# Performance work log

Hardware: AMD Instinct MI355X
Metric: run time of the kernel (lower is better)

## Reference

```python
import jax, jax.numpy as jnp
import numpy as np

H = 16          # num_heads
TOP_K = 2
LN_EPS = 1e-5


def setup_inputs() -> dict:
    key = jax.random.key(0)
    ks = jax.random.split(key, 8)
    B, S, E, NE = 2, 1024, 1024, 8
    w = lambda k, shp: jax.random.normal(k, shp, dtype=jnp.float32) * 0.02
    return {
        "x": jax.random.normal(ks[0], (B, S, E), dtype=jnp.float32),
        "rW1": w(ks[1], (E // 2, E)),
        "rb1": jnp.zeros((E // 2,), jnp.float32),
        "ln_g": jnp.ones((E // 2,), jnp.float32),
        "ln_b": jnp.zeros((E // 2,), jnp.float32),
        "rW2": w(ks[2], (NE, E // 2)),
        "rb2": jnp.zeros((NE,), jnp.float32),
        "qW": w(ks[3], (NE, E, E)),
        "qb": jnp.zeros((NE, E), jnp.float32),
        "kW": w(ks[4], (NE, E, E)),
        "kb": jnp.zeros((NE, E), jnp.float32),
        "vW": w(ks[5], (NE, E, E)),
        "vb": jnp.zeros((NE, E), jnp.float32),
        "oW": w(ks[6], (NE, E, E)),
        "ob": jnp.zeros((NE, E), jnp.float32),
    }


def reference(x, rW1, rb1, ln_g, ln_b, rW2, rb2, qW, qb, kW, kb, vW, vb, oW, ob):
    B, S, E = x.shape
    NE = qW.shape[0]
    Dh = E // H
    scale = 1.0 / jnp.sqrt(jnp.asarray(Dh, x.dtype))

    # ---- router: Linear -> LayerNorm -> ReLU -> Linear ----
    h = x @ rW1.T + rb1                       # [B,S,E/2]
    mu = h.mean(-1, keepdims=True)
    var = ((h - mu) ** 2).mean(-1, keepdims=True)
    h = (h - mu) * jax.lax.rsqrt(var + LN_EPS) * ln_g + ln_b
    h = jax.nn.relu(h)
    logits = h @ rW2.T + rb2                  # [B,S,NE]
    probs = jax.nn.softmax(logits, axis=-1)

    # ---- top-k gating, renormalized, scattered to dense expert mask ----
    tp, ti = jax.lax.top_k(probs, TOP_K)      # [B,S,K]
    tp = tp / tp.sum(-1, keepdims=True)
    expert_mask = (jax.nn.one_hot(ti, NE, dtype=probs.dtype) * tp[..., None]).sum(-2)  # [B,S,NE]
    gates = jnp.moveaxis(expert_mask, -1, 0)  # [NE,B,S]

    # ---- every expert attends over all tokens; outputs gated and summed ----
    def expert_step(acc, params):
        qw, qb_, kw, kb_, vw, vb_, ow, ob_, g = params
        q = (x @ qw.T + qb_).reshape(B, S, H, Dh).transpose(0, 2, 1, 3)  # [B,H,S,Dh]
        k = (x @ kw.T + kb_).reshape(B, S, H, Dh).transpose(0, 2, 1, 3)
        v = (x @ vw.T + vb_).reshape(B, S, H, Dh).transpose(0, 2, 1, 3)
        scores = jnp.einsum("bhqd,bhkd->bhqk", q, k) * scale
        p = jax.nn.softmax(scores, axis=-1)
        o = jnp.einsum("bhqk,bhkd->bhqd", p, v)
        o = o.transpose(0, 2, 1, 3).reshape(B, S, E) @ ow.T + ob_
        return acc + o * g[..., None], None

    out, _ = jax.lax.scan(expert_step, jnp.zeros_like(x),
                          (qW, qb, kW, kb, vW, vb, oW, ob, gates))
    return out
```

## Files before the change

kernel.cpp:

```cpp
#include <hip/hip_runtime.h>
#include <hip/hip_bf16.h>

typedef unsigned short u16;
typedef unsigned int u32;
typedef __bf16 bf16x8 __attribute__((ext_vector_type(8)));
typedef float f32x4 __attribute__((ext_vector_type(4)));

__device__ __forceinline__ u16 f2bf(float f) {
  union { float f; unsigned u; } v; v.f = f;
  unsigned r = v.u + 0x7fffu + ((v.u >> 16) & 1u);
  return (u16)(r >> 16);
}

__device__ __forceinline__ f32x4 mfma16(bf16x8 a, bf16x8 b, f32x4 c) {
  return __builtin_amdgcn_mfma_f32_16x16x32_bf16(a, b, c, 0, 0, 0);
}

__device__ __forceinline__ void gl_lds16(const u16* g, u16* l) {
  __builtin_amdgcn_global_load_lds(
      (const __attribute__((address_space(1))) u32*)g,
      (__attribute__((address_space(3))) u32*)l, 16, 0, 0);
}

__global__ __launch_bounds__(256) void cvt_x_kernel(const float* __restrict__ x,
                                                    u16* __restrict__ xb,
                                                    u32* __restrict__ lists) {
  size_t i = (size_t)blockIdx.x * 256 + threadIdx.x;
  if (i < 32784) lists[i] = 0;
  float4 v = reinterpret_cast<const float4*>(x)[i];
  unsigned long long pk = (unsigned long long)f2bf(v.x) |
                          ((unsigned long long)f2bf(v.y) << 16) |
                          ((unsigned long long)f2bf(v.z) << 32) |
                          ((unsigned long long)f2bf(v.w) << 48);
  *reinterpret_cast<unsigned long long*>(xb + i * 4) = pk;
}

__global__ __launch_bounds__(256) void cvt_w_kernel(
    const float* __restrict__ qW, const float* __restrict__ kW,
    const float* __restrict__ vW, const float* __restrict__ oW,
    u16* __restrict__ wb_qkv, u16* __restrict__ wb_o) {
  const size_t nqkv4 = (size_t)8 * 3 * 262144;
  const size_t total = nqkv4 + (size_t)8 * 262144;
  for (size_t i = (size_t)blockIdx.x * 256 + threadIdx.x; i < total;
       i += (size_t)gridDim.x * 256) {
    const float* src; u16* dst;
    if (i < nqkv4) {
      size_t elem = i * 4;
      size_t blk = elem >> 20;
      size_t el = blk / 3, ty = blk % 3;
      const float* W = (ty == 0 ? qW : (ty == 1 ? kW : vW));
      src = W + el * 1048576 + (elem & 1048575);
      dst = wb_qkv + elem;
    } else {
      size_t elem = (i - nqkv4) * 4;
      size_t el = elem >> 20;
      src = oW + el * 1048576 + (elem & 1048575);
      dst = wb_o + elem;
    }
    float4 v = *reinterpret_cast<const float4*>(src);
    unsigned long long pk = (unsigned long long)f2bf(v.x) |
                            ((unsigned long long)f2bf(v.y) << 16) |
                            ((unsigned long long)f2bf(v.z) << 32) |
                            ((unsigned long long)f2bf(v.w) << 48);
    *reinterpret_cast<unsigned long long*>(dst) = pk;
  }
}

__global__ __launch_bounds__(256) void router_gemm1(
    const float* __restrict__ x, const float* __restrict__ rW1,
    const float* __restrict__ rb1, float* __restrict__ hbuf) {
  __shared__ float aT[32][72];
  __shared__ float bT[32][72];
  int t = threadIdx.x;
  int tx = t & 15, ty = t >> 4;
  int m0 = blockIdx.x * 64, n0 = blockIdx.y * 64;
  float acc[4][4];
#pragma unroll
  for (int i = 0; i < 4; ++i)
#pragma unroll
    for (int j = 0; j < 4; ++j) acc[i][j] = 0.f;
  const float* Ab = x + (size_t)m0 * 1024;
  const float* Bb = rW1 + (size_t)n0 * 1024;
  int r = t >> 2, c8 = (t & 3) * 8;
  for (int k0 = 0; k0 < 1024; k0 += 32) {
    float4 av0 = *reinterpret_cast<const float4*>(Ab + (size_t)r * 1024 + k0 + c8);
    float4 av1 = *reinterpret_cast<const float4*>(Ab + (size_t)r * 1024 + k0 + c8 + 4);
    float4 bv0 = *reinterpret_cast<const float4*>(Bb + (size_t)r * 1024 + k0 + c8);
    float4 bv1 = *reinterpret_cast<const float4*>(Bb + (size_t)r * 1024 + k0 + c8 + 4);
    aT[c8 + 0][r] = av0.x; aT[c8 + 1][r] = av0.y; aT[c8 + 2][r] = av0.z; aT[c8 + 3][r] = av0.w;
    aT[c8 + 4][r] = av1.x; aT[c8 + 5][r] = av1.y; aT[c8 + 6][r] = av1.z; aT[c8 + 7][r] = av1.w;
    bT[c8 + 0][r] = bv0.x; bT[c8 + 1][r] = bv0.y; bT[c8 + 2][r] = bv0.z; bT[c8 + 3][r] = bv0.w;
    bT[c8 + 4][r] = bv1.x; bT[c8 + 5][r] = bv1.y; bT[c8 + 6][r] = bv1.z; bT[c8 + 7][r] = bv1.w;
    __syncthreads();
#pragma unroll
    for (int kk = 0; kk < 32; ++kk) {
      float4 a = *reinterpret_cast<const float4*>(&aT[kk][ty * 4]);
      float4 b = *reinterpret_cast<const float4*>(&bT[kk][tx * 4]);
      float aa[4] = {a.x, a.y, a.z, a.w};
      float bb[4] = {b.x, b.y, b.z, b.w};
#pragma unroll
      for (int i = 0; i < 4; ++i)
#pragma unroll
        for (int j = 0; j < 4; ++j) acc[i][j] += aa[i] * bb[j];
    }
    __syncthreads();
  }
#pragma unroll
  for (int i = 0; i < 4; ++i) {
    int row = m0 + ty * 4 + i;
#pragma unroll
    for (int j = 0; j < 4; ++j) {
      int col = n0 + tx * 4 + j;
      hbuf[(size_t)row * 512 + col] = acc[i][j] + rb1[col];
    }
  }
}

__global__ __launch_bounds__(64) void router_finish(
    const float* __restrict__ hbuf, const float* __restrict__ ln_g,
    const float* __restrict__ ln_b, const float* __restrict__ rW2,
    const float* __restrict__ rb2,
    u32* __restrict__ tok_list, float* __restrict__ gate_list,
    u32* __restrict__ cnt, u32* __restrict__ inv) {
  int tok = blockIdx.x, lane = threadIdx.x;
  const float* hr = hbuf + (size_t)tok * 512;
  float4 v0 = *reinterpret_cast<const float4*>(hr + lane * 8);
  float4 v1 = *reinterpret_cast<const float4*>(hr + lane * 8 + 4);
  float hv[8] = {v0.x, v0.y, v0.z, v0.w, v1.x, v1.y, v1.z, v1.w};
  float s = 0.f;
#pragma unroll
  for (int j = 0; j < 8; ++j) s += hv[j];
#pragma unroll
  for (int m = 1; m < 64; m <<= 1) s += __shfl_xor(s, m);
  float mu = s * (1.0f / 512.0f);
  float s2 = 0.f;
#pragma unroll
  for (int j = 0; j < 8; ++j) { float d = hv[j] - mu; s2 += d * d; }
#pragma unroll
  for (int m = 1; m < 64; m <<= 1) s2 += __shfl_xor(s2, m);
  float rstd = 1.0f / sqrtf(s2 * (1.0f / 512.0f) + 1e-5f);
#pragma unroll
  for (int j = 0; j < 8; ++j) {
    float tv = (hv[j] - mu) * rstd * ln_g[lane * 8 + j] + ln_b[lane * 8 + j];
    hv[j] = fmaxf(tv, 0.0f);
  }
  float logit[8];
#pragma unroll
  for (int n = 0; n < 8; ++n) {
    const float* wr = rW2 + (size_t)n * 512 + lane * 8;
    float p = 0.f;
#pragma unroll
    for (int j = 0; j < 8; ++j) p += hv[j] * wr[j];
#pragma unroll
    for (int m = 1; m < 64; m <<= 1) p += __shfl_xor(p, m);
    logit[n] = p + rb2[n];
  }
  int i1 = 0; float l1 = logit[0];
#pragma unroll
  for (int n = 1; n < 8; ++n) if (logit[n] > l1) { l1 = logit[n]; i1 = n; }
  int i2 = -1; float l2 = -3.4e38f;
#pragma unroll
  for (int n = 0; n < 8; ++n) if (n != i1 && logit[n] > l2) { l2 = logit[n]; i2 = n; }
  float e2 = __expf(l2 - l1);
  float g1 = 1.0f / (1.0f + e2);
  float g2 = e2 * g1;
  if (lane == 0) {
    int b = tok >> 10, sq = tok & 1023;
    int p1 = i1 * 2 + b;
    u32 pos1 = atomicAdd(&cnt[p1], 1u);
    tok_list[p1 * 1024 + pos1] = (u32)sq;
    gate_list[p1 * 1024 + pos1] = g1;
    inv[tok * 2 + 0] = ((u32)p1 << 10) | pos1;
    int p2 = i2 * 2 + b;
    u32 pos2 = atomicAdd(&cnt[p2], 1u);
    tok_list[p2 * 1024 + pos2] = (u32)sq;
    gate_list[p2 * 1024 + pos2] = g2;
    inv[tok * 2 + 1] = ((u32)p2 << 10) | pos2;
  }
}

__device__ __forceinline__ void stage8(
    const u16* aS0, const u16* aS1, const u16* aS2, const u16* aS3,
    const u16* bS0, const u16* bS1, const u16* bS2, const u16* bS3,
    int k0, u16* aL, u16* bL, int w) {
  gl_lds16(aS0 + k0, aL + (32 * w + 0) * 64);
  gl_lds16(aS1 + k0, aL + (32 * w + 8) * 64);
  gl_lds16(aS2 + k0, aL + (32 * w + 16) * 64);
  gl_lds16(aS3 + k0, aL + (32 * w + 24) * 64);
  gl_lds16(bS0 + k0, bL + (32 * w + 0) * 64);
  gl_lds16(bS1 + k0, bL + (32 * w + 8) * 64);
  gl_lds16(bS2 + k0, bL + (32 * w + 16) * 64);
  gl_lds16(bS3 + k0, bL + (32 * w + 24) * 64);
}

__device__ __forceinline__ void gemm_mainloop_p(
    const u16* aS0, const u16* aS1, const u16* aS2, const u16* aS3,
    const u16* bS0, const u16* bS1, const u16* bS2, const u16* bS3,
    int K, u16* aL0, u16* bL0, u16* aL1, u16* bL1, f32x4 acc[4][4]) {
  const int t = threadIdx.x;
  const int w = t >> 6, lane = t & 63;
  const int wm = (w >> 1) * 64, wn = (w & 1) * 64;
  const int lr = lane & 15, lg = lane >> 4;
  const int T = K >> 6;
  stage8(aS0, aS1, aS2, aS3, bS0, bS1, bS2, bS3, 0, aL0, bL0, w);
  __syncthreads();
  for (int tt = 0; tt < T; ++tt) {
    u16* aC = (tt & 1) ? aL1 : aL0;
    u16* bC = (tt & 1) ? bL1 : bL0;
    if (tt + 1 < T) {
      u16* aN = (tt & 1) ? aL0 : aL1;
      u16* bN = (tt & 1) ? bL0 : bL1;
      stage8(aS0, aS1, aS2, aS3, bS0, bS1, bS2, bS3, (tt + 1) << 6, aN, bN, w);
    }
    __builtin_amdgcn_s_setprio(1);
#pragma unroll
    for (int kk = 0; kk < 2; ++kk) {
      bf16x8 af[4], bfr[4];
#pragma unroll
      for (int i = 0; i < 4; ++i) {
        int ra = wm + i * 16 + lr;
        af[i] = *reinterpret_cast<const bf16x8*>(aC + ra * 64 + (((kk * 4 + lg) ^ (ra & 7)) << 3));
        int rb = wn + i * 16 + lr;
        bfr[i] = *reinterpret_cast<const bf16x8*>(bC + rb * 64 + (((kk * 4 + lg) ^ (rb & 7)) << 3));
      }
#pragma unroll
      for (int mi = 0; mi < 4; ++mi)
#pragma unroll
        for (int ni = 0; ni < 4; ++ni)
          acc[mi][ni] = mfma16(af[mi], bfr[ni], acc[mi][ni]);
    }
    __builtin_amdgcn_s_setprio(0);
    __syncthreads();
  }
}

__device__ __forceinline__ void stage6(
    const u16* aS0, const u16* aS1,
    const u16* bS0, const u16* bS1, const u16* bS2, const u16* bS3,
    int k0, u16* aL, u16* bL, int w) {
  gl_lds16(aS0 + k0, aL + (16 * w + 0) * 64);
  gl_lds16(aS1 + k0, aL + (16 * w + 8) * 64);
  gl_lds16(bS0 + k0, bL + (32 * w + 0) * 64);
  gl_lds16(bS1 + k0, bL + (32 * w + 8) * 64);
  gl_lds16(bS2 + k0, bL + (32 * w + 16) * 64);
  gl_lds16(bS3 + k0, bL + (32 * w + 24) * 64);
}

__device__ __forceinline__ void gemm_mainloop64(
    const u16* aS0, const u16* aS1,
    const u16* bS0, const u16* bS1, const u16* bS2, const u16* bS3,
    int K, u16* aL0, u16* bL0, u16* aL1, u16* bL1, f32x4 acc[4][2]) {
  const int t = threadIdx.x;
  const int w = t >> 6, lane = t & 63;
  const int lr = lane & 15, lg = lane >> 4;
  const int T = K >> 6;
  stage6(aS0, aS1, bS0, bS1, bS2, bS3, 0, aL0, bL0, w);
  __syncthreads();
  for (int tt = 0; tt < T; ++tt) {
    u16* aC = (tt & 1) ? aL1 : aL0;
    u16* bC = (tt & 1) ? bL1 : bL0;
    if (tt + 1 < T) {
      u16* aN = (tt & 1) ? aL0 : aL1;
      u16* bN = (tt & 1) ? bL0 : bL1;
      stage6(aS0, aS1, bS0, bS1, bS2, bS3, (tt + 1) << 6, aN, bN, w);
    }
    __builtin_amdgcn_s_setprio(1);
#pragma unroll
    for (int kk = 0; kk < 2; ++kk) {
      bf16x8 af[4], bfr[2];
#pragma unroll
      for (int i = 0; i < 4; ++i) {
        int ra = i * 16 + lr;
        af[i] = *reinterpret_cast<const bf16x8*>(aC + ra * 64 + (((kk * 4 + lg) ^ (ra & 7)) << 3));
      }
#pragma unroll
      for (int j = 0; j < 2; ++j) {
        int rb = w * 32 + j * 16 + lr;
        bfr[j] = *reinterpret_cast<const bf16x8*>(bC + rb * 64 + (((kk * 4 + lg) ^ (rb & 7)) << 3));
      }
#pragma unroll
      for (int mi = 0; mi < 4; ++mi)
#pragma unroll
        for (int ni = 0; ni < 2; ++ni)
          acc[mi][ni] = mfma16(af[mi], bfr[ni], acc[mi][ni]);
    }
    __builtin_amdgcn_s_setprio(0);
    __syncthreads();
  }
}

__global__ __launch_bounds__(256) void kv_gemm_kernel(
    const u16* __restrict__ xb, const u16* __restrict__ wb_qkv,
    const float* __restrict__ kb, const float* __restrict__ vb,
    u16* __restrict__ kbuf, u16* __restrict__ vtbuf) {
  __shared__ u16 lds[32768];
  int orig = blockIdx.x;
  int wgid = (orig & 7) * 256 + (orig >> 3);
  int e = wgid >> 8, r = wgid & 255;
  int ty = r >> 7, rr = r & 127;
  const int t = threadIdx.x, w = t >> 6, lane = t & 63;
  const int rloc = lane >> 3, cloc = lane & 7;
  const int sc8 = (cloc ^ rloc) * 8;
  const u16 *A, *B;
  int mblk, nblk;
  if (ty == 0) {
    mblk = rr >> 3; nblk = rr & 7;
    A = xb + (size_t)mblk * 128 * 1024;
    B = wb_qkv + (size_t)(e * 3 + 1) * 1048576 + (size_t)nblk * 128 * 1024;
  } else {
    mblk = rr & 7; nblk = rr >> 3;
    A = wb_qkv + (size_t)(e * 3 + 2) * 1048576 + (size_t)mblk * 128 * 1024;
    B = xb + (size_t)nblk * 128 * 1024;
  }
  f32x4 acc[4][4];
#pragma unroll
  for (int i = 0; i < 4; ++i)
#pragma unroll
    for (int j = 0; j < 4; ++j) { f32x4 z = {0.f, 0.f, 0.f, 0.f}; acc[i][j] = z; }
  gemm_mainloop_p(
      A + (size_t)(32 * w + 0 + rloc) * 1024 + sc8, A + (size_t)(32 * w + 8 + rloc) * 1024 + sc8,
      A + (size_t)(32 * w + 16 + rloc) * 1024 + sc8, A + (size_t)(32 * w + 24 + rloc) * 1024 + sc8,
      B + (size_t)(32 * w + 0 + rloc) * 1024 + sc8, B + (size_t)(32 * w + 8 + rloc) * 1024 + sc8,
      B + (size_t)(32 * w + 16 + rloc) * 1024 + sc8, B + (size_t)(32 * w + 24 + rloc) * 1024 + sc8,
      1024, lds, lds + 8192, lds + 16384, lds + 24576, acc);
  const int wm = (w >> 1) * 64, wn = (w & 1) * 64;
  const int lr = lane & 15, lg = lane >> 4;
  if (ty == 0) {
    const float* bias = kb + (size_t)e * 1024 + nblk * 128;
    u16* Cb = kbuf + ((size_t)e * 2048 + (size_t)mblk * 128) * 1024 + nblk * 128;
#pragma unroll
    for (int ni = 0; ni < 4; ++ni) {
      int lcol = wn + ni * 16 + lr;
      float bv = bias[lcol];
#pragma unroll
      for (int mi = 0; mi < 4; ++mi)
#pragma unroll
        for (int rg = 0; rg < 4; ++rg) {
          int lrow = wm + mi * 16 + lg * 4 + rg;
          Cb[(size_t)lrow * 1024 + lcol] = f2bf(acc[mi][ni][rg] + bv);
        }
    }
  } else {
    const float* bias = vb + (size_t)e * 1024 + mblk * 128;
    int bb = nblk >> 3, nn = nblk & 7;
    u16* Cb = vtbuf + ((size_t)(e * 2 + bb) * 1024 + (size_t)mblk * 128) * 1024 + nn * 128;
#pragma unroll
    for (int ni = 0; ni < 4; ++ni) {
      int lcol = wn + ni * 16 + lr;
#pragma unroll
      for (int mi = 0; mi < 4; ++mi)
#pragma unroll
        for (int rg = 0; rg < 4; ++rg) {
          int lrow = wm + mi * 16 + lg * 4 + rg;
          Cb[(size_t)lrow * 1024 + lcol] = f2bf(acc[mi][ni][rg] + bias[lrow]);
        }
    }
  }
}

__global__ __launch_bounds__(256) void q_gemm_kernel(
    const u16* __restrict__ xb, const u16* __restrict__ wb_qkv,
    const float* __restrict__ qb, const u32* __restrict__ tok_list,
    const u32* __restrict__ cnt, u16* __restrict__ qc) {
  __shared__ u16 lds[24576];
  int nblk = blockIdx.x, mt = blockIdx.y, p = blockIdx.z;
  int c = (int)cnt[p];
  if (mt * 64 >= c) return;
  int e = p >> 1, b = p & 1;
  const int t = threadIdx.x, w = t >> 6, lane = t & 63;
  const int rloc = lane >> 3, cloc = lane & 7;
  const int sc8 = (cloc ^ rloc) * 8;
  const u32* tl = tok_list + p * 1024 + mt * 64 + 16 * w + rloc;
  int t0 = (int)(tl[0] & 1023), t1 = (int)(tl[8] & 1023);
  const u16* Ab = xb + (size_t)b * 1024 * 1024 + sc8;
  const u16* B = wb_qkv + (size_t)(e * 3) * 1048576 + (size_t)nblk * 128 * 1024;
  f32x4 acc[4][2];
#pragma unroll
  for (int i = 0; i < 4; ++i)
#pragma unroll
    for (int j = 0; j < 2; ++j) { f32x4 z = {0.f, 0.f, 0.f, 0.f}; acc[i][j] = z; }
  gemm_mainloop64(
      Ab + (size_t)t0 * 1024, Ab + (size_t)t1 * 1024,
      B + (size_t)(32 * w + 0 + rloc) * 1024 + sc8, B + (size_t)(32 * w + 8 + rloc) * 1024 + sc8,
      B + (size_t)(32 * w + 16 + rloc) * 1024 + sc8, B + (size_t)(32 * w + 24 + rloc) * 1024 + sc8,
      1024, lds, lds + 8192, lds + 4096, lds + 16384, acc);
  const int lr = lane & 15, lg = lane >> 4;
  const float* bias = qb + (size_t)e * 1024 + nblk * 128;
  u16* Cb = qc + ((size_t)p * 1024 + (size_t)mt * 64) * 1024 + nblk * 128;
#pragma unroll
  for (int ni = 0; ni < 2; ++ni) {
    int lcol = w * 32 + ni * 16 + lr;
    float bv = bias[lcol];
#pragma unroll
    for (int mi = 0; mi < 4; ++mi)
#pragma unroll
      for (int rg = 0; rg < 4; ++rg) {
        int lrow = mi * 16 + lg * 4 + rg;
        Cb[(size_t)lrow * 1024 + lcol] = f2bf(acc[mi][ni][rg] + bv);
      }
  }
}

__global__ __launch_bounds__(256) void attn_kernel(
    const u16* __restrict__ qc, const u16* __restrict__ kbuf,
    const u16* __restrict__ vtbuf, const u32* __restrict__ cnt,
    u16* __restrict__ oc) {
  __shared__ u16 Kl[2][4096];
  __shared__ u16 Vtl[2][4096];
  __shared__ u16 Pl[4096];
  int h = blockIdx.x;
  int p = blockIdx.y >> 3, lt = blockIdx.y & 7;
  int c = (int)cnt[p];
  if (lt * 64 >= c) return;
  int e = p >> 1, b = p & 1;
  const u16* Qb = qc + ((size_t)p * 1024 + (size_t)lt * 64) * 1024 + h * 64;
  const u16* Kg = kbuf + ((size_t)e * 2048 + (size_t)b * 1024) * 1024 + h * 64;
  const u16* Vtg = vtbuf + ((size_t)(e * 2 + b) * 1024 + (size_t)h * 64) * 1024;
  u16* Og = oc + ((size_t)p * 1024 + (size_t)lt * 64) * 1024 + h * 64;
  const int t = threadIdx.x, w = t >> 6, lane = t & 63;
  const int lr = lane & 15, lg = lane >> 4;
  const int rloc = lane >> 3, kc = lane & 7;

#define STAGE_ATTN(IT, KB, VB)                                                   \
  {                                                                              \
    int kv0_ = (IT) * 64;                                                        \
    _Pragma("unroll")                                                            \
    for (int r_ = 0; r_ < 2; ++r_) {                                             \
      int row_ = 16 * w + 8 * r_ + rloc;                                         \
      gl_lds16(Kg + (size_t)(kv0_ + row_) * 1024 + (kc ^ (row_ & 7)) * 8,        \
               (KB) + (16 * w + 8 * r_) * 64);                                   \
      gl_lds16(Vtg + (size_t)row_ * 1024 + kv0_ + (kc ^ (row_ & 7)) * 8,         \
               (VB) + (16 * w + 8 * r_) * 64);                                   \
    }                                                                            \
  }

  STAGE_ATTN(0, Kl[0], Vtl[0]);

  bf16x8 qa0 = *reinterpret_cast<const bf16x8*>(Qb + (size_t)(w * 16 + lr) * 1024 + lg * 8);
  bf16x8 qa1 = *reinterpret_cast<const bf16x8*>(Qb + (size_t)(w * 16 + lr) * 1024 + 32 + lg * 8);

  f32x4 oacc[4];
  float mrun[4], lsum[4];
#pragma unroll
  for (int i = 0; i < 4; ++i) {
    f32x4 z = {0.f, 0.f, 0.f, 0.f}; oacc[i] = z; mrun[i] = -3.4e38f; lsum[i] = 0.f;
  }
  __syncthreads();

  for (int it = 0; it < 16; ++it) {
    const int cur = it & 1;
    const u16* Kc = Kl[cur];
    const u16* Vc = Vtl[cur];
    if (it + 1 < 16) STAGE_ATTN(it + 1, Kl[cur ^ 1], Vtl[cur ^ 1]);
    f32x4 sv[4];
    __builtin_amdgcn_s_setprio(1);
#pragma unroll
    for (int nt = 0; nt < 4; ++nt) {
      f32x4 z = {0.f, 0.f, 0.f, 0.f};
#pragma unroll
      for (int kk = 0; kk < 2; ++kk) {
        int rk = nt * 16 + lr;
        bf16x8 kf = *reinterpret_cast<const bf16x8*>(Kc + rk * 64 + (((kk * 4 + lg) ^ (rk & 7)) << 3));
        z = mfma16(kk ? qa1 : qa0, kf, z);
      }
      sv[nt] = z * 0.125f;
    }
    __builtin_amdgcn_s_setprio(0);
#pragma unroll
    for (int rg = 0; rg < 4; ++rg) {
      float tm = fmaxf(fmaxf(sv[0][rg], sv[1][rg]), fmaxf(sv[2][rg], sv[3][rg]));
#pragma unroll
      for (int mm = 1; mm < 16; mm <<= 1) tm = fmaxf(tm, __shfl_xor(tm, mm));
      float mn = fmaxf(mrun[rg], tm);
      float al = __expf(mrun[rg] - mn);
      mrun[rg] = mn;
      lsum[rg] *= al;
#pragma unroll
      for (int nt = 0; nt < 4; ++nt) oacc[nt][rg] *= al;
    }
#pragma unroll
    for (int nt = 0; nt < 4; ++nt) {
#pragma unroll
      for (int rg = 0; rg < 4; ++rg) {
        float pv = __expf(sv[nt][rg] - mrun[rg]);
        lsum[rg] += pv;
        int prow = lg * 4 + rg;
        Pl[w * 1024 + prow * 64 + ((nt * 16 + lr) ^ ((prow & 7) << 3))] = f2bf(pv);
      }
    }
    __builtin_amdgcn_s_setprio(1);
#pragma unroll
    for (int kk = 0; kk < 2; ++kk) {
      bf16x8 pf = *reinterpret_cast<const bf16x8*>(
          Pl + w * 1024 + lr * 64 + (((kk * 4 + lg) ^ (lr & 7)) << 3));
#pragma unroll
      for (int nt = 0; nt < 4; ++nt) {
        int rv = nt * 16 + lr;
        bf16x8 vf = *reinterpret_cast<const bf16x8*>(Vc + rv * 64 + (((kk * 4 + lg) ^ (rv & 7)) << 3));
        oacc[nt] = mfma16(pf, vf, oacc[nt]);
      }
    }
    __builtin_amdgcn_s_setprio(0);
    __syncthreads();
  }
#pragma unroll
  for (int rg = 0; rg < 4; ++rg) {
#pragma unroll
    for (int mm = 1; mm < 16; mm <<= 1) lsum[rg] += __shfl_xor(lsum[rg], mm);
    float inv = 1.0f / lsum[rg];
#pragma unroll
    for (int nt = 0; nt < 4; ++nt)
      Og[(size_t)(w * 16 + lg * 4 + rg) * 1024 + nt * 16 + lr] = f2bf(oacc[nt][rg] * inv);
  }
#undef STAGE_ATTN
}

__global__ __launch_bounds__(256) void oproj_kernel(
    const u16* __restrict__ oc, const u16* __restrict__ wb_o,
    const u32* __restrict__ cnt, float* __restrict__ projc) {
  __shared__ u16 lds[24576];
  int nblk = blockIdx.x, mt = blockIdx.y, p = blockIdx.z;
  int c = (int)cnt[p];
  if (mt * 64 >= c) return;
  int e = p >> 1;
  const int t = threadIdx.x, w = t >> 6, lane = t & 63;
  const int rloc = lane >> 3, cloc = lane & 7;
  const int sc8 = (cloc ^ rloc) * 8;
  const u16* A = oc + ((size_t)p * 1024 + (size_t)mt * 64) * 1024;
  const u16* B = wb_o + (size_t)e * 1048576 + (size_t)nblk * 128 * 1024;
  f32x4 acc[4][2];
#pragma unroll
  for (int i = 0; i < 4; ++i)
#pragma unroll
    for (int j = 0; j < 2; ++j) { f32x4 z = {0.f, 0.f, 0.f, 0.f}; acc[i][j] = z; }
  gemm_mainloop64(
      A + (size_t)(16 * w + 0 + rloc) * 1024 + sc8, A + (size_t)(16 * w + 8 + rloc) * 1024 + sc8,
      B + (size_t)(32 * w + 0 + rloc) * 1024 + sc8, B + (size_t)(32 * w + 8 + rloc) * 1024 + sc8,
      B + (size_t)(32 * w + 16 + rloc) * 1024 + sc8, B + (size_t)(32 * w + 24 + rloc) * 1024 + sc8,
      1024, lds, lds + 8192, lds + 4096, lds + 16384, acc);
  const int lr = lane & 15, lg = lane >> 4;
  float* Pb = projc + ((size_t)p * 1024 + (size_t)mt * 64) * 1024 + nblk * 128;
#pragma unroll
  for (int mi = 0; mi < 4; ++mi)
#pragma unroll
    for (int rg = 0; rg < 4; ++rg) {
      int lrow = mi * 16 + lg * 4 + rg;
#pragma unroll
      for (int ni = 0; ni < 2; ++ni) {
        int lcol = w * 32 + ni * 16 + lr;
        Pb[(size_t)lrow * 1024 + lcol] = acc[mi][ni][rg];
      }
    }
}

__global__ __launch_bounds__(256) void merge_out(
    const float* __restrict__ projc, const float* __restrict__ ob,
    const float* __restrict__ gate_list, const u32* __restrict__ inv,
    float* __restrict__ out) {
  int tok = blockIdx.x;
  int c4 = threadIdx.x * 4;
  u32 i1 = inv[tok * 2], i2 = inv[tok * 2 + 1];
  int idx1 = (int)(i1 >> 10) * 1024 + (int)(i1 & 1023);
  int idx2 = (int)(i2 >> 10) * 1024 + (int)(i2 & 1023);
  float g1 = gate_list[idx1], g2 = gate_list[idx2];
  int e1 = (int)(i1 >> 11), e2 = (int)(i2 >> 11);
  float4 a = *reinterpret_cast<const float4*>(projc + (size_t)idx1 * 1024 + c4);
  float4 bvec = *reinterpret_cast<const float4*>(projc + (size_t)idx2 * 1024 + c4);
  float4 o1 = *reinterpret_cast<const float4*>(ob + (size_t)e1 * 1024 + c4);
  float4 o2 = *reinterpret_cast<const float4*>(ob + (size_t)e2 * 1024 + c4);
  float4 r;
  r.x = g1 * (a.x + o1.x) + g2 * (bvec.x + o2.x);
  r.y = g1 * (a.y + o1.y) + g2 * (bvec.y + o2.y);
  r.z = g1 * (a.z + o1.z) + g2 * (bvec.z + o2.z);
  r.w = g1 * (a.w + o1.w) + g2 * (bvec.w + o2.w);
  *reinterpret_cast<float4*>(out + (size_t)tok * 1024 + c4) = r;
}

extern "C" void kernel_launch(void* const* d_in, const int* in_sizes, int n_in,
                              void* d_out, int out_size, void* d_ws, size_t ws_size,
                              hipStream_t stream) {
  const float* x    = (const float*)d_in[0];
  const float* rW1  = (const float*)d_in[1];
  const float* rb1  = (const float*)d_in[2];
  const float* ln_g = (const float*)d_in[3];
  const float* ln_b = (const float*)d_in[4];
  const float* rW2  = (const float*)d_in[5];
  const float* rb2  = (const float*)d_in[6];
  const float* qW   = (const float*)d_in[7];
  const float* qb   = (const float*)d_in[8];
  const float* kW   = (const float*)d_in[9];
  const float* kb   = (const float*)d_in[10];
  const float* vW   = (const float*)d_in[11];
  const float* vb   = (const float*)d_in[12];
  const float* oW   = (const float*)d_in[13];
  const float* ob   = (const float*)d_in[14];
  float* out = (float*)d_out;

  const size_t need = 50331648ull + 16777216ull + 67108864ull + 33554432ull +
                      33554432ull + 4194304ull + 147520ull;
  if (ws_size < need) return;
  char* pp = (char*)d_ws;
  u16* wb_qkv = (u16*)pp; pp += 50331648ull;
  u16* wb_o   = (u16*)pp; pp += 16777216ull;
  u16* kbuf   = (u16*)pp; pp += 33554432ull;
  u16* vtbuf  = (u16*)pp; pp += 33554432ull;
  u16* qc     = (u16*)pp; pp += 33554432ull;
  u16* oc     = (u16*)pp; pp += 33554432ull;
  u16* xb     = (u16*)pp; pp += 4194304ull;
  u32* lists  = (u32*)pp;
  u32* tok_list    = lists;
  float* gate_list = (float*)(lists + 16384);
  u32* cnt         = lists + 32768;
  u32* inv         = lists + 32784;
  float* hbuf  = (float*)qc;
  float* projc = (float*)kbuf;

  cvt_x_kernel<<<dim3(2048), dim3(256), 0, stream>>>(x, xb, lists);
  cvt_w_kernel<<<dim3(2048), dim3(256), 0, stream>>>(qW, kW, vW, oW, wb_qkv, wb_o);
  router_gemm1<<<dim3(32, 8), dim3(256), 0, stream>>>(x, rW1, rb1, hbuf);
  router_finish<<<dim3(2048), dim3(64), 0, stream>>>(hbuf, ln_g, ln_b, rW2, rb2,
                                                     tok_list, gate_list, cnt, inv);
  kv_gemm_kernel<<<dim3(2048), dim3(256), 0, stream>>>(xb, wb_qkv, kb, vb, kbuf, vtbuf);
  q_gemm_kernel<<<dim3(8, 16, 16), dim3(256), 0, stream>>>(xb, wb_qkv, qb, tok_list, cnt, qc);
  attn_kernel<<<dim3(16, 128), dim3(256), 0, stream>>>(qc, kbuf, vtbuf, cnt, oc);
  oproj_kernel<<<dim3(8, 16, 16), dim3(256), 0, stream>>>(oc, wb_o, cnt, projc);
  merge_out<<<dim3(2048), dim3(256), 0, stream>>>(projc, ob, gate_list, inv, out);
}
```

Baseline: 480.8 us.

## Merge prep kernels and fuse K/V and Q projection GEMMs into single launches

The x conversion, weight conversion and router first GEMM are combined into one launch, with each role chosen by block-index range. The K/V GEMM and the routed Q GEMM are likewise merged into one grid. This removes launch gaps and kernel-boundary tails and lets independent work overlap on the GPU. The cost is a larger shared-memory footprint for the Q blocks, which now allocate the K/V kernel's 64KB LDS instead of 48KB. The weight-conversion loop also runs with 1024 blocks instead of 2048.

```diff
diff --git a/kernel.cpp b/kernel.cpp
--- a/kernel.cpp
+++ b/kernel.cpp
@@ -22,58 +22,58 @@
       (__attribute__((address_space(3))) u32*)l, 16, 0, 0);
 }
 
-__global__ __launch_bounds__(256) void cvt_x_kernel(const float* __restrict__ x,
-                                                    u16* __restrict__ xb,
-                                                    u32* __restrict__ lists) {
-  size_t i = (size_t)blockIdx.x * 256 + threadIdx.x;
-  if (i < 32784) lists[i] = 0;
-  float4 v = reinterpret_cast<const float4*>(x)[i];
-  unsigned long long pk = (unsigned long long)f2bf(v.x) |
-                          ((unsigned long long)f2bf(v.y) << 16) |
-                          ((unsigned long long)f2bf(v.z) << 32) |
-                          ((unsigned long long)f2bf(v.w) << 48);
-  *reinterpret_cast<unsigned long long*>(xb + i * 4) = pk;
-}
-
-__global__ __launch_bounds__(256) void cvt_w_kernel(
+__global__ __launch_bounds__(256) void prep_kernel(
+    const float* __restrict__ x, u16* __restrict__ xb, u32* __restrict__ lists,
     const float* __restrict__ qW, const float* __restrict__ kW,
     const float* __restrict__ vW, const float* __restrict__ oW,
-    u16* __restrict__ wb_qkv, u16* __restrict__ wb_o) {
-  const size_t nqkv4 = (size_t)8 * 3 * 262144;
-  const size_t total = nqkv4 + (size_t)8 * 262144;
-  for (size_t i = (size_t)blockIdx.x * 256 + threadIdx.x; i < total;
-       i += (size_t)gridDim.x * 256) {
-    const float* src; u16* dst;
-    if (i < nqkv4) {
-      size_t elem = i * 4;
-      size_t blk = elem >> 20;
-      size_t el = blk / 3, ty = blk % 3;
-      const float* W = (ty == 0 ? qW : (ty == 1 ? kW : vW));
-      src = W + el * 1048576 + (elem & 1048575);
-      dst = wb_qkv + elem;
-    } else {
-      size_t elem = (i - nqkv4) * 4;
-      size_t el = elem >> 20;
-      src = oW + el * 1048576 + (elem & 1048575);
-      dst = wb_o + elem;
-    }
-    float4 v = *reinterpret_cast<const float4*>(src);
+    u16* __restrict__ wb_qkv, u16* __restrict__ wb_o,
+    const float* __restrict__ rW1, const float* __restrict__ rb1,
+    float* __restrict__ hbuf) {
+  __shared__ float smem[2 * 32 * 72];
+  const int b = blockIdx.x, t = threadIdx.x;
+  if (b < 2048) {
+    size_t i = (size_t)b * 256 + t;
+    if (i < 32784) lists[i] = 0;
+    float4 v = reinterpret_cast<const float4*>(x)[i];
     unsigned long long pk = (unsigned long long)f2bf(v.x) |
                             ((unsigned long long)f2bf(v.y) << 16) |
                             ((unsigned long long)f2bf(v.z) << 32) |
                             ((unsigned long long)f2bf(v.w) << 48);
-    *reinterpret_cast<unsigned long long*>(dst) = pk;
-  }
-}
-
-__global__ __launch_bounds__(256) void router_gemm1(
-    const float* __restrict__ x, const float* __restrict__ rW1,
-    const float* __restrict__ rb1, float* __restrict__ hbuf) {
-  __shared__ float aT[32][72];
-  __shared__ float bT[32][72];
-  int t = threadIdx.x;
+    *reinterpret_cast<unsigned long long*>(xb + i * 4) = pk;
+    return;
+  }
+  if (b < 3072) {
+    const size_t nqkv4 = (size_t)8 * 3 * 262144;
+    const size_t total = nqkv4 + (size_t)8 * 262144;
+    for (size_t i = (size_t)(b - 2048) * 256 + t; i < total; i += 1024 * 256) {
+      const float* src; u16* dst;
+      if (i < nqkv4) {
+        size_t elem = i * 4;
+        size_t blk = elem >> 20;
+        size_t el = blk / 3, ty = blk % 3;
+        const float* W = (ty == 0 ? qW : (ty == 1 ? kW : vW));
+        src = W + el * 1048576 + (elem & 1048575);
+        dst = wb_qkv + elem;
+      } else {
+        size_t elem = (i - nqkv4) * 4;
+        size_t el = elem >> 20;
+        src = oW + el * 1048576 + (elem & 1048575);
+        dst = wb_o + elem;
+      }
+      float4 v = *reinterpret_cast<const float4*>(src);
+      unsigned long long pk = (unsigned long long)f2bf(v.x) |
+                              ((unsigned long long)f2bf(v.y) << 16) |
+                              ((unsigned long long)f2bf(v.z) << 32) |
+                              ((unsigned long long)f2bf(v.w) << 48);
+      *reinterpret_cast<unsigned long long*>(dst) = pk;
+    }
+    return;
+  }
+  float (*aT)[72] = reinterpret_cast<float(*)[72]>(smem);
+  float (*bT)[72] = reinterpret_cast<float(*)[72]>(smem + 32 * 72);
+  int bid = b - 3072;
   int tx = t & 15, ty = t >> 4;
-  int m0 = blockIdx.x * 64, n0 = blockIdx.y * 64;
+  int m0 = (bid & 31) * 64, n0 = (bid >> 5) * 64;
   float acc[4][4];
 #pragma unroll
   for (int i = 0; i < 4; ++i)
@@ -95,13 +95,13 @@
 #pragma unroll
     for (int kk = 0; kk < 32; ++kk) {
       float4 a = *reinterpret_cast<const float4*>(&aT[kk][ty * 4]);
-      float4 b = *reinterpret_cast<const float4*>(&bT[kk][tx * 4]);
+      float4 bb = *reinterpret_cast<const float4*>(&bT[kk][tx * 4]);
       float aa[4] = {a.x, a.y, a.z, a.w};
-      float bb[4] = {b.x, b.y, b.z, b.w};
+      float bv[4] = {bb.x, bb.y, bb.z, bb.w};
 #pragma unroll
       for (int i = 0; i < 4; ++i)
 #pragma unroll
-        for (int j = 0; j < 4; ++j) acc[i][j] += aa[i] * bb[j];
+        for (int j = 0; j < 4; ++j) acc[i][j] += aa[i] * bv[j];
     }
     __syncthreads();
   }
@@ -289,115 +289,110 @@
   }
 }
 
-__global__ __launch_bounds__(256) void kv_gemm_kernel(
+__global__ __launch_bounds__(256) void kvq_gemm_kernel(
     const u16* __restrict__ xb, const u16* __restrict__ wb_qkv,
     const float* __restrict__ kb, const float* __restrict__ vb,
-    u16* __restrict__ kbuf, u16* __restrict__ vtbuf) {
+    const float* __restrict__ qb, const u32* __restrict__ tok_list,
+    const u32* __restrict__ cnt,
+    u16* __restrict__ kbuf, u16* __restrict__ vtbuf, u16* __restrict__ qc) {
   __shared__ u16 lds[32768];
-  int orig = blockIdx.x;
-  int wgid = (orig & 7) * 256 + (orig >> 3);
-  int e = wgid >> 8, r = wgid & 255;
-  int ty = r >> 7, rr = r & 127;
   const int t = threadIdx.x, w = t >> 6, lane = t & 63;
   const int rloc = lane >> 3, cloc = lane & 7;
   const int sc8 = (cloc ^ rloc) * 8;
-  const u16 *A, *B;
-  int mblk, nblk;
-  if (ty == 0) {
-    mblk = rr >> 3; nblk = rr & 7;
-    A = xb + (size_t)mblk * 128 * 1024;
-    B = wb_qkv + (size_t)(e * 3 + 1) * 1048576 + (size_t)nblk * 128 * 1024;
+  const int lr = lane & 15, lg = lane >> 4;
+  if (blockIdx.x < 2048) {
+    int orig = blockIdx.x;
+    int wgid = (orig & 7) * 256 + (orig >> 3);
+    int e = wgid >> 8, r = wgid & 255;
+    int ty = r >> 7, rr = r & 127;
+    const u16 *A, *B;
+    int mblk, nblk;
+    if (ty == 0) {
+      mblk = rr >> 3; nblk = rr & 7;
+      A = xb + (size_t)mblk * 128 * 1024;
+      B = wb_qkv + (size_t)(e * 3 + 1) * 1048576 + (size_t)nblk * 128 * 1024;
+    } else {
+      mblk = rr & 7; nblk = rr >> 3;
+      A = wb_qkv + (size_t)(e * 3 + 2) * 1048576 + (size_t)mblk * 128 * 1024;
+      B = xb + (size_t)nblk * 128 * 1024;
+    }
+    f32x4 acc[4][4];
+#pragma unroll
+    for (int i = 0; i < 4; ++i)
+#pragma unroll
+      for (int j = 0; j < 4; ++j) { f32x4 z = {0.f, 0.f, 0.f, 0.f}; acc[i][j] = z; }
+    gemm_mainloop_p(
+        A + (size_t)(32 * w + 0 + rloc) * 1024 + sc8, A + (size_t)(32 * w + 8 + rloc) * 1024 + sc8,
+        A + (size_t)(32 * w + 16 + rloc) * 1024 + sc8, A + (size_t)(32 * w + 24 + rloc) * 1024 + sc8,
+        B + (size_t)(32 * w + 0 + rloc) * 1024 + sc8, B + (size_t)(32 * w + 8 + rloc) * 1024 + sc8,
+        B + (size_t)(32 * w + 16 + rloc) * 1024 + sc8, B + (size_t)(32 * w + 24 + rloc) * 1024 + sc8,
+        1024, lds, lds + 8192, lds + 16384, lds + 24576, acc);
+    const int wm = (w >> 1) * 64, wn = (w & 1) * 64;
+    if (ty == 0) {
+      const float* bias = kb + (size_t)e * 1024 + nblk * 128;
+      u16* Cb = kbuf + ((size_t)e * 2048 + (size_t)mblk * 128) * 1024 + nblk * 128;
+#pragma unroll
+      for (int ni = 0; ni < 4; ++ni) {
+        int lcol = wn + ni * 16 + lr;
+        float bv = bias[lcol];
+#pragma unroll
+        for (int mi = 0; mi < 4; ++mi)
+#pragma unroll
+          for (int rg = 0; rg < 4; ++rg) {
+            int lrow = wm + mi * 16 + lg * 4 + rg;
+            Cb[(size_t)lrow * 1024 + lcol] = f2bf(acc[mi][ni][rg] + bv);
+          }
+      }
+    } else {
+      const float* bias = vb + (size_t)e * 1024 + mblk * 128;
+      int bb = nblk >> 3, nn = nblk & 7;
+      u16* Cb = vtbuf + ((size_t)(e * 2 + bb) * 1024 + (size_t)mblk * 128) * 1024 + nn * 128;
+#pragma unroll
+      for (int ni = 0; ni < 4; ++ni) {
+        int lcol = wn + ni * 16 + lr;
+#pragma unroll
+        for (int mi = 0; mi < 4; ++mi)
+#pragma unroll
+          for (int rg = 0; rg < 4; ++rg) {
+            int lrow = wm + mi * 16 + lg * 4 + rg;
+            Cb[(size_t)lrow * 1024 + lcol] = f2bf(acc[mi][ni][rg] + bias[lrow]);
+          }
+      }
+    }
   } else {
-    mblk = rr & 7; nblk = rr >> 3;
-    A = wb_qkv + (size_t)(e * 3 + 2) * 1048576 + (size_t)mblk * 128 * 1024;
-    B = xb + (size_t)nblk * 128 * 1024;
-  }
-  f32x4 acc[4][4];
-#pragma unroll
-  for (int i = 0; i < 4; ++i)
-#pragma unroll
-    for (int j = 0; j < 4; ++j) { f32x4 z = {0.f, 0.f, 0.f, 0.f}; acc[i][j] = z; }
-  gemm_mainloop_p(
-      A + (size_t)(32 * w + 0 + rloc) * 1024 + sc8, A + (size_t)(32 * w + 8 + rloc) * 1024 + sc8,
-      A + (size_t)(32 * w + 16 + rloc) * 1024 + sc8, A + (size_t)(32 * w + 24 + rloc) * 1024 + sc8,
-      B + (size_t)(32 * w + 0 + rloc) * 1024 + sc8, B + (size_t)(32 * w + 8 + rloc) * 1024 + sc8,
-      B + (size_t)(32 * w + 16 + rloc) * 1024 + sc8, B + (size_t)(32 * w + 24 + rloc) * 1024 + sc8,
-      1024, lds, lds + 8192, lds + 16384, lds + 24576, acc);
-  const int wm = (w >> 1) * 64, wn = (w & 1) * 64;
-  const int lr = lane & 15, lg = lane >> 4;
-  if (ty == 0) {
-    const float* bias = kb + (size_t)e * 1024 + nblk * 128;
-    u16* Cb = kbuf + ((size_t)e * 2048 + (size_t)mblk * 128) * 1024 + nblk * 128;
-#pragma unroll
-    for (int ni = 0; ni < 4; ++ni) {
-      int lcol = wn + ni * 16 + lr;
+    int bid = blockIdx.x - 2048;
+    int nblk = bid & 7, mt = (bid >> 3) & 15, p = bid >> 7;
+    int c = (int)cnt[p];
+    if (mt * 64 >= c) return;
+    int e = p >> 1, b = p & 1;
+    const u32* tl = tok_list + p * 1024 + mt * 64 + 16 * w + rloc;
+    int t0 = (int)(tl[0] & 1023), t1 = (int)(tl[8] & 1023);
+    const u16* Ab = xb + (size_t)b * 1024 * 1024 + sc8;
+    const u16* B = wb_qkv + (size_t)(e * 3) * 1048576 + (size_t)nblk * 128 * 1024;
+    f32x4 acc[4][2];
+#pragma unroll
+    for (int i = 0; i < 4; ++i)
+#pragma unroll
+      for (int j = 0; j < 2; ++j) { f32x4 z = {0.f, 0.f, 0.f, 0.f}; acc[i][j] = z; }
+    gemm_mainloop64(
+        Ab + (size_t)t0 * 1024, Ab + (size_t)t1 * 1024,
+        B + (size_t)(32 * w + 0 + rloc) * 1024 + sc8, B + (size_t)(32 * w + 8 + rloc) * 1024 + sc8,
+        B + (size_t)(32 * w + 16 + rloc) * 1024 + sc8, B + (size_t)(32 * w + 24 + rloc) * 1024 + sc8,
+        1024, lds, lds + 8192, lds + 4096, lds + 16384, acc);
+    const float* bias = qb + (size_t)e * 1024 + nblk * 128;
+    u16* Cb = qc + ((size_t)p * 1024 + (size_t)mt * 64) * 1024 + nblk * 128;
+#pragma unroll
+    for (int ni = 0; ni < 2; ++ni) {
+      int lcol = w * 32 + ni * 16 + lr;
       float bv = bias[lcol];
 #pragma unroll
       for (int mi = 0; mi < 4; ++mi)
 #pragma unroll
         for (int rg = 0; rg < 4; ++rg) {
-          int lrow = wm + mi * 16 + lg * 4 + rg;
+          int lrow = mi * 16 + lg * 4 + rg;
           Cb[(size_t)lrow * 1024 + lcol] = f2bf(acc[mi][ni][rg] + bv);
         }
     }
-  } else {
-    const float* bias = vb + (size_t)e * 1024 + mblk * 128;
-    int bb = nblk >> 3, nn = nblk & 7;
-    u16* Cb = vtbuf + ((size_t)(e * 2 + bb) * 1024 + (size_t)mblk * 128) * 1024 + nn * 128;
-#pragma unroll
-    for (int ni = 0; ni < 4; ++ni) {
-      int lcol = wn + ni * 16 + lr;
-#pragma unroll
-      for (int mi = 0; mi < 4; ++mi)
-#pragma unroll
-        for (int rg = 0; rg < 4; ++rg) {
-          int lrow = wm + mi * 16 + lg * 4 + rg;
-          Cb[(size_t)lrow * 1024 + lcol] = f2bf(acc[mi][ni][rg] + bias[lrow]);
-        }
-    }
-  }
-}
-
-__global__ __launch_bounds__(256) void q_gemm_kernel(
-    const u16* __restrict__ xb, const u16* __restrict__ wb_qkv,
-    const float* __restrict__ qb, const u32* __restrict__ tok_list,
-    const u32* __restrict__ cnt, u16* __restrict__ qc) {
-  __shared__ u16 lds[24576];
-  int nblk = blockIdx.x, mt = blockIdx.y, p = blockIdx.z;
-  int c = (int)cnt[p];
-  if (mt * 64 >= c) return;
-  int e = p >> 1, b = p & 1;
-  const int t = threadIdx.x, w = t >> 6, lane = t & 63;
-  const int rloc = lane >> 3, cloc = lane & 7;
-  const int sc8 = (cloc ^ rloc) * 8;
-  const u32* tl = tok_list + p * 1024 + mt * 64 + 16 * w + rloc;
-  int t0 = (int)(tl[0] & 1023), t1 = (int)(tl[8] & 1023);
-  const u16* Ab = xb + (size_t)b * 1024 * 1024 + sc8;
-  const u16* B = wb_qkv + (size_t)(e * 3) * 1048576 + (size_t)nblk * 128 * 1024;
-  f32x4 acc[4][2];
-#pragma unroll
-  for (int i = 0; i < 4; ++i)
-#pragma unroll
-    for (int j = 0; j < 2; ++j) { f32x4 z = {0.f, 0.f, 0.f, 0.f}; acc[i][j] = z; }
-  gemm_mainloop64(
-      Ab + (size_t)t0 * 1024, Ab + (size_t)t1 * 1024,
-      B + (size_t)(32 * w + 0 + rloc) * 1024 + sc8, B + (size_t)(32 * w + 8 + rloc) * 1024 + sc8,
-      B + (size_t)(32 * w + 16 + rloc) * 1024 + sc8, B + (size_t)(32 * w + 24 + rloc) * 1024 + sc8,
-      1024, lds, lds + 8192, lds + 4096, lds + 16384, acc);
-  const int lr = lane & 15, lg = lane >> 4;
-  const float* bias = qb + (size_t)e * 1024 + nblk * 128;
-  u16* Cb = qc + ((size_t)p * 1024 + (size_t)mt * 64) * 1024 + nblk * 128;
-#pragma unroll
-  for (int ni = 0; ni < 2; ++ni) {
-    int lcol = w * 32 + ni * 16 + lr;
-    float bv = bias[lcol];
-#pragma unroll
-    for (int mi = 0; mi < 4; ++mi)
-#pragma unroll
-      for (int rg = 0; rg < 4; ++rg) {
-        int lrow = mi * 16 + lg * 4 + rg;
-        Cb[(size_t)lrow * 1024 + lcol] = f2bf(acc[mi][ni][rg] + bv);
-      }
   }
 }
 
@@ -615,13 +610,12 @@
   float* hbuf  = (float*)qc;
   float* projc = (float*)kbuf;
 
-  cvt_x_kernel<<<dim3(2048), dim3(256), 0, stream>>>(x, xb, lists);
-  cvt_w_kernel<<<dim3(2048), dim3(256), 0, stream>>>(qW, kW, vW, oW, wb_qkv, wb_o);
-  router_gemm1<<<dim3(32, 8), dim3(256), 0, stream>>>(x, rW1, rb1, hbuf);
+  prep_kernel<<<dim3(3328), dim3(256), 0, stream>>>(
+      x, xb, lists, qW, kW, vW, oW, wb_qkv, wb_o, rW1, rb1, hbuf);
   router_finish<<<dim3(2048), dim3(64), 0, stream>>>(hbuf, ln_g, ln_b, rW2, rb2,
                                                      tok_list, gate_list, cnt, inv);
-  kv_gemm_kernel<<<dim3(2048), dim3(256), 0, stream>>>(xb, wb_qkv, kb, vb, kbuf, vtbuf);
-  q_gemm_kernel<<<dim3(8, 16, 16), dim3(256), 0, stream>>>(xb, wb_qkv, qb, tok_list, cnt, qc);
+  kvq_gemm_kernel<<<dim3(4096), dim3(256), 0, stream>>>(
+      xb, wb_qkv, kb, vb, qb, tok_list, cnt, kbuf, vtbuf, qc);
   attn_kernel<<<dim3(16, 128), dim3(256), 0, stream>>>(qc, kbuf, vtbuf, cnt, oc);
   oproj_kernel<<<dim3(8, 16, 16), dim3(256), 0, stream>>>(oc, wb_o, cnt, projc);
   merge_out<<<dim3(2048), dim3(256), 0, stream>>>(projc, ob, gate_list, inv, out);
```

Result: no change. 484.2 us (+0.7%).
